# Performance work log

Hardware: AMD Instinct MI355X
Metric: run time of the kernel (lower is better)

The kernel has to match this reference:

```python
import jax, jax.numpy as jnp
import numpy as np

NUM_HEADS = 16


def rotate_half(x):
    half = x.shape[-1] // 2
    return jnp.concatenate((-x[..., half:], x[..., :half]), axis=-1)


def rope_tables(seq_len, head_dim, dtype=jnp.float32):
    inv_freq = 1.0 / (10000.0 ** (jnp.arange(0, head_dim, 2, dtype=jnp.float32) / head_dim))
    t = jnp.arange(seq_len, dtype=jnp.float32)
    freqs = jnp.outer(t, inv_freq)                 # [S, hd/2]
    emb = jnp.concatenate((freqs, freqs), axis=-1)  # [S, hd]
    return jnp.cos(emb).astype(dtype), jnp.sin(emb).astype(dtype)


def setup_inputs() -> dict:
    key = jax.random.key(0)
    k1, k2, k3 = jax.random.split(key, 3)
    B, S, D = 2, 2048, 1024
    x = jax.random.normal(k1, (B, S, D), dtype=jnp.float32)
    # causal lower-triangular mask, broadcast over batch/heads
    mask = jnp.tril(jnp.ones((S, S), dtype=bool))[None, None, :, :]
    w_qkv = jax.random.normal(k2, (3 * D, D), dtype=jnp.float32) * (D ** -0.5)
    w_out = jax.random.normal(k3, (D, D), dtype=jnp.float32) * (D ** -0.5)
    return {"x": x, "mask": mask, "w_qkv": w_qkv, "w_out": w_out}


def reference(x, mask, w_qkv, w_out):
    B, S, D = x.shape
    H = NUM_HEADS
    hd = D // H
    scale = hd ** -0.5

    qkv = jnp.einsum('bsd,ed->bse', x, w_qkv)          # [B, S, 3D]
    q, k, v = jnp.split(qkv, 3, axis=-1)

    def split(t):
        return t.reshape(B, S, H, hd).transpose(0, 2, 1, 3)  # [B, H, S, hd]

    q, k, v = split(q), split(k), split(v)

    cos, sin = rope_tables(S, hd, x.dtype)             # [S, hd]
    cos = cos[None, None]
    sin = sin[None, None]
    q = q * cos + rotate_half(q) * sin
    k = k * cos + rotate_half(k) * sin

    attn = jnp.einsum('bhqd,bhkd->bhqk', q, k) * scale  # [B, H, S, S]
    attn = jnp.where(mask, attn, jnp.float32(-jnp.inf).astype(attn.dtype))
    attn = jax.nn.softmax(attn, axis=-1)
    out = jnp.einsum('bhqk,bhkd->bhqd', attn, v)        # [B, H, S, hd]
    out = out.transpose(0, 2, 1, 3).reshape(B, S, D)
    return jnp.einsum('bsd,ed->bse', out, w_out)
```

## Files before the change

kernel.cpp:

```cpp
#include <hip/hip_runtime.h>
#include <hip/hip_bf16.h>

typedef __attribute__((ext_vector_type(8))) __bf16 bf16x8;
typedef __attribute__((ext_vector_type(4))) __bf16 bf16x4;
typedef __attribute__((ext_vector_type(2))) __bf16 bf16x2;
typedef __attribute__((ext_vector_type(4))) float f32x4;
typedef __attribute__((ext_vector_type(16))) float f32x16;

#define SEQ 2048
#define NH 16
#define HD 64
#define DMODEL 1024
#define BATCH 2
#define MTOT 4096
#define NSLOT 72

#if __has_builtin(__builtin_amdgcn_exp2f)
#define EXP2(x) __builtin_amdgcn_exp2f(x)
#else
#define EXP2(x) exp2f(x)
#endif
#define MFMA32(a, b, c) __builtin_amdgcn_mfma_f32_32x32x16_bf16(a, b, c, 0, 0, 0)

__device__ __forceinline__ void gl_lds16(const void* g, void* l) {
    __builtin_amdgcn_global_load_lds(
        (const __attribute__((address_space(1))) void*)(uintptr_t)g,
        (__attribute__((address_space(3))) void*)(uintptr_t)l,
        16, 0, 0);
}

__device__ __forceinline__ unsigned pk2(float x, float y) {
    union { bf16x2 h; unsigned u; } c;
    c.h = bf16x2{ (__bf16)x, (__bf16)y };
    return c.u;
}

__constant__ int4 FITEM[80] = {
    {31,0,16,68},{31,16,32,69},{31,32,48,70},{31,48,64,71},
    {23,0,16,37},{23,16,32,38},{23,32,48,39},
    {15,0,16,14},{15,16,32,15},
    {30,15,31,65},{30,46,62,67},
    {22,30,46,36},
    {7,0,16,-1},
    {29,0,15,60},{29,15,30,61},{29,30,45,62},{29,45,60,63},
    {30,0,15,64},{30,31,46,66},
    {22,0,15,34},{22,15,30,35},
    {21,14,29,32},{21,29,44,33},
    {28,14,29,57},{28,43,58,59},
    {14,0,15,12},{14,15,30,13},
    {27,0,14,52},{27,14,28,53},{27,28,42,54},{27,42,56,55},
    {28,0,14,56},{28,29,43,58},
    {20,0,14,28},{20,14,28,29},{20,28,42,30},
    {21,0,14,31},
    {26,13,27,49},{26,40,54,51},
    {19,26,40,27},
    {13,0,14,10},{13,14,28,11},
    {6,0,14,-1},
    {25,0,13,44},{25,13,26,45},{25,26,39,46},{25,39,52,47},
    {26,0,13,48},{26,27,40,50},
    {24,12,25,41},{24,37,50,43},
    {19,0,13,25},{19,13,26,26},
    {18,12,25,23},{18,25,38,24},
    {12,0,13,8},{12,13,26,9},
    {24,0,12,40},{24,25,37,42},
    {17,0,12,19},{17,12,24,20},{17,24,36,21},
    {18,0,12,22},
    {16,22,34,18},
    {11,0,12,6},{11,12,24,7},
    {5,0,12,-1},
    {16,0,11,16},{16,11,22,17},
    {10,0,11,4},{10,11,22,5},
    {9,0,10,2},{9,10,20,3},
    {4,0,10,-1},
    {8,0,9,0},{8,9,18,1},
    {3,0,8,-1},{2,0,6,-1},{1,0,4,-1},{0,0,2,-1}
};

__global__ __launch_bounds__(256) void cast3(const float4* __restrict__ x,
                                             const float4* __restrict__ wq,
                                             const float4* __restrict__ wo,
                                             __bf16* __restrict__ xb,
                                             __bf16* __restrict__ wqb,
                                             __bf16* __restrict__ wob) {
    const int NX  = 1024 * 1024;
    const int NWQ = 768 * 1024;
    const int NTOT = NX + NWQ + 256 * 1024;
    int i = blockIdx.x * 256 + threadIdx.x;
    if (i >= NTOT) return;
    float4 v; __bf16* dst; int j;
    if (i < NX)            { j = i;            v = x[j];  dst = xb;  }
    else if (i < NX + NWQ) { j = i - NX;       v = wq[j]; dst = wqb; }
    else                   { j = i - NX - NWQ; v = wo[j]; dst = wob; }
    bf16x4 o = { (__bf16)v.x, (__bf16)v.y, (__bf16)v.z, (__bf16)v.w };
    *(bf16x4*)(dst + (size_t)j * 4) = o;
}

__global__ __launch_bounds__(256) void gemm_qkv(const __bf16* __restrict__ A,
                                                const __bf16* __restrict__ Bt,
                                                __bf16* __restrict__ Qp,
                                                char* __restrict__ K2,
                                                char* __restrict__ V2) {
    const int K = 1024;
    __shared__ __bf16 sA[128 * 64];
    __shared__ __bf16 sB[128 * 64];
    const int tid = threadIdx.x, lane = tid & 63, wave = tid >> 6;
    const int lrow = lane & 15, quad = lane >> 4;
    const int m0 = blockIdx.y * 128, n0 = blockIdx.x * 128;
    const int wm = wave >> 1, wn = wave & 1;

    const __bf16* ap[4]; const __bf16* bp[4]; int ldso[4];
#pragma unroll
    for (int i = 0; i < 4; ++i) {
        int r0 = i * 32 + wave * 8;
        int row = r0 + (lane >> 3);
        int cg = (lane & 7) ^ (row & 7);
        ap[i] = A + (size_t)(m0 + row) * K + cg * 8;
        bp[i] = Bt + (size_t)(n0 + row) * K + cg * 8;
        ldso[i] = r0 * 128;
    }
    int arow[4], brow[4];
#pragma unroll
    for (int i = 0; i < 4; ++i) {
        arow[i] = wm * 64 + i * 16 + lrow;
        brow[i] = wn * 64 + i * 16 + lrow;
    }

    f32x4 z = {0.f, 0.f, 0.f, 0.f};
    f32x4 acc[4][4];
#pragma unroll
    for (int i = 0; i < 4; ++i)
#pragma unroll
        for (int j = 0; j < 4; ++j) acc[i][j] = z;

    char* sAb = (char*)sA; char* sBb = (char*)sB;
    for (int k0 = 0; k0 < K; k0 += 64) {
#pragma unroll
        for (int i = 0; i < 4; ++i) gl_lds16(ap[i] + k0, sAb + ldso[i]);
#pragma unroll
        for (int i = 0; i < 4; ++i) gl_lds16(bp[i] + k0, sBb + ldso[i]);
        __syncthreads();
#pragma unroll
        for (int ks = 0; ks < 2; ++ks) {
            bf16x8 af[4], bfr[4];
#pragma unroll
            for (int i = 0; i < 4; ++i)
                af[i] = *(const bf16x8*)(sAb + arow[i] * 128 +
                                         (((ks * 4 + quad) ^ (arow[i] & 7)) << 4));
#pragma unroll
            for (int i = 0; i < 4; ++i)
                bfr[i] = *(const bf16x8*)(sBb + brow[i] * 128 +
                                          (((ks * 4 + quad) ^ (brow[i] & 7)) << 4));
#pragma unroll
            for (int i = 0; i < 4; ++i)
#pragma unroll
                for (int j = 0; j < 4; ++j)
                    acc[i][j] = __builtin_amdgcn_mfma_f32_16x16x32_bf16(
                        af[i], bfr[j], acc[i][j], 0, 0, 0);
        }
        __syncthreads();
    }

    const int nt = blockIdx.x;
    const int sec = nt >> 3;
    const int b = m0 >> 11;
    const int s0b = m0 & (SEQ - 1);
    const int h = (nt & 7) * 2 + wn;
    const int bh = b * NH + h;

    if (sec < 2) {
        const float scale = sec ? 1.0f : 0.18033688011112042f;
        char* Kb = K2 + (size_t)bh * 262144;
        float invf0 = 0.15915494309189535f *
                      exp2f(-(float)lrow * 0.4152410118609203f);
        float invf1 = invf0 * 0.01f;
#pragma unroll
        for (int i = 0; i < 4; ++i) {
            int srow0 = s0b + wm * 64 + i * 16 + quad * 4;
#pragma unroll
            for (int j = 0; j < 2; ++j) {
                float invf = j ? invf1 : invf0;
                int hdlo = j * 16 + lrow;
#pragma unroll
                for (int r = 0; r < 4; ++r) {
                    int s = srow0 + r;
                    float rev = (float)s * invf;
                    float fr = rev - floorf(rev);
                    float sn = __builtin_amdgcn_sinf(fr);
                    float cs = __builtin_amdgcn_cosf(fr);
                    float lo = acc[i][j][r], hi = acc[i][j + 2][r];
                    float olo = (lo * cs - hi * sn) * scale;
                    float ohi = (hi * cs + lo * sn) * scale;
                    if (sec == 0) {
                        size_t base = ((size_t)bh * SEQ + s) * HD + hdlo;
                        Qp[base] = (__bf16)olo;
                        Qp[base + 32] = (__bf16)ohi;
                    } else {
                        char* kt = Kb + (s >> 5) * 4096 + (s & 31) * 16 +
                                   ((lrow >> 3) & 1) * 512 + (lrow & 7) * 2;
                        *(__bf16*)(kt + j * 1024) = (__bf16)olo;
                        *(__bf16*)(kt + (j + 2) * 1024) = (__bf16)ohi;
                    }
                }
            }
        }
    } else {
        char* Vb = V2 + (size_t)bh * 262144;
#pragma unroll
        for (int i = 0; i < 4; ++i) {
            int srow0 = s0b + wm * 64 + i * 16 + quad * 4;
            int kb = srow0 >> 4, ko = srow0 & 15;
            int slot0 = ((ko >> 2) & 1) * 8 + (ko >> 3) * 4;
#pragma unroll
            for (int j = 0; j < 4; ++j) {
                int ch = j * 16 + lrow;
                bf16x4 wv = { (__bf16)acc[i][j][0], (__bf16)acc[i][j][1],
                              (__bf16)acc[i][j][2], (__bf16)acc[i][j][3] };
                *(bf16x4*)(Vb + kb * 2048 + ch * 32 + slot0 * 2) = wv;
            }
        }
    }
}

__global__ __launch_bounds__(256) void gemm_bt(const __bf16* __restrict__ A,
                                               const __bf16* __restrict__ Bt,
                                               float* __restrict__ Cf,
                                               int M, int N, int K) {
    __shared__ __bf16 sA[128 * 64];
    __shared__ __bf16 sB[128 * 64];
    const int tid = threadIdx.x, lane = tid & 63, wave = tid >> 6;
    const int lrow = lane & 15, quad = lane >> 4;
    const int m0 = blockIdx.y * 128, n0 = blockIdx.x * 128;
    const int wm = wave >> 1, wn = wave & 1;

    const __bf16* ap[4]; const __bf16* bp[4]; int ldso[4];
#pragma unroll
    for (int i = 0; i < 4; ++i) {
        int r0 = i * 32 + wave * 8;
        int row = r0 + (lane >> 3);
        int cg = (lane & 7) ^ (row & 7);
        ap[i] = A + (size_t)(m0 + row) * K + cg * 8;
        bp[i] = Bt + (size_t)(n0 + row) * K + cg * 8;
        ldso[i] = r0 * 128;
    }
    int arow[4], brow[4];
#pragma unroll
    for (int i = 0; i < 4; ++i) {
        arow[i] = wm * 64 + i * 16 + lrow;
        brow[i] = wn * 64 + i * 16 + lrow;
    }

    f32x4 z = {0.f, 0.f, 0.f, 0.f};
    f32x4 acc[4][4];
#pragma unroll
    for (int i = 0; i < 4; ++i)
#pragma unroll
        for (int j = 0; j < 4; ++j) acc[i][j] = z;

    char* sAb = (char*)sA; char* sBb = (char*)sB;
    for (int k0 = 0; k0 < K; k0 += 64) {
#pragma unroll
        for (int i = 0; i < 4; ++i) gl_lds16(ap[i] + k0, sAb + ldso[i]);
#pragma unroll
        for (int i = 0; i < 4; ++i) gl_lds16(bp[i] + k0, sBb + ldso[i]);
        __syncthreads();
#pragma unroll
        for (int ks = 0; ks < 2; ++ks) {
            bf16x8 af[4], bfr[4];
#pragma unroll
            for (int i = 0; i < 4; ++i)
                af[i] = *(const bf16x8*)(sAb + arow[i] * 128 +
                                         (((ks * 4 + quad) ^ (arow[i] & 7)) << 4));
#pragma unroll
            for (int i = 0; i < 4; ++i)
                bfr[i] = *(const bf16x8*)(sBb + brow[i] * 128 +
                                          (((ks * 4 + quad) ^ (brow[i] & 7)) << 4));
#pragma unroll
            for (int i = 0; i < 4; ++i)
#pragma unroll
                for (int j = 0; j < 4; ++j)
                    acc[i][j] = __builtin_amdgcn_mfma_f32_16x16x32_bf16(
                        af[i], bfr[j], acc[i][j], 0, 0, 0);
        }
        __syncthreads();
    }
#pragma unroll
    for (int i = 0; i < 4; ++i)
#pragma unroll
        for (int j = 0; j < 4; ++j)
#pragma unroll
            for (int r = 0; r < 4; ++r) {
                int row = m0 + wm * 64 + i * 16 + quad * 4 + r;
                int col = n0 + wn * 64 + j * 16 + lrow;
                Cf[(size_t)row * N + col] = acc[i][j][r];
            }
}

__global__ __launch_bounds__(64) void flash_attn(const __bf16* __restrict__ Qp,
                                                 const char* __restrict__ K2,
                                                 const char* __restrict__ V2,
                                                 __bf16* __restrict__ Aout,
                                                 __bf16* __restrict__ Opart,
                                                 float* __restrict__ Lpart) {
    const int lane = threadIdx.x;
    const int ql = lane & 31, half = lane >> 5;
    const int bh = blockIdx.x;
    const int4 it = FITEM[blockIdx.y];
    const int s = it.x, t0 = it.y, t1 = it.z, slot = it.w;
    const int b = bh >> 4, hh = bh & 15;

    const __bf16* qb = Qp + ((size_t)bh * SEQ + s * 64 + ql) * HD + half * 8;
    bf16x8 qf0[4], qf1[4];
#pragma unroll
    for (int kc = 0; kc < 4; ++kc) {
        qf0[kc] = *(const bf16x8*)(qb + kc * 16);
        qf1[kc] = *(const bf16x8*)(qb + 32 * HD + kc * 16);
    }
    const char* Kb = K2 + (size_t)bh * 262144 + half * 512 + ql * 16;
    const char* Vb = V2 + (size_t)bh * 262144 + ql * 32 + half * 16;

    f32x16 zz = {0.f};
    f32x16 oA0 = zz, oA1 = zz, oB0 = zz, oB1 = zz;
    float lA = 0.f, lB = 0.f;
    const int dA = 2 * s, dB = 2 * s + 1;
    const int thr = ql - 4 * half;

    auto STEP = [&](int t, const bf16x8* kf, bf16x8* kn) {
        bf16x8 vf[2][2];
#pragma unroll
        for (int lo = 0; lo < 2; ++lo) {
            const char* vp = Vb + (t * 2 + lo) * 2048;
            vf[lo][0] = *(const bf16x8*)(vp);
            vf[lo][1] = *(const bf16x8*)(vp + 1024);
        }
        if (t + 1 < t1) {
            const char* kt = Kb + (t + 1) * 4096;
#pragma unroll
            for (int kc = 0; kc < 4; ++kc)
                kn[kc] = *(const bf16x8*)(kt + kc * 1024);
        }
        const bool do0 = (t != dB);
        f32x16 st0 = zz, st1 = zz;
        if (do0) {
#pragma unroll
            for (int kc = 0; kc < 4; ++kc)
                st0 = MFMA32(kf[kc], qf0[kc], st0);
        }
#pragma unroll
        for (int kc = 0; kc < 4; ++kc)
            st1 = MFMA32(kf[kc], qf1[kc], st1);

        if (do0) {
#pragma unroll
            for (int i = 0; i < 16; ++i) st0[i] = EXP2(st0[i]);
            if (t == dA) {
#pragma unroll
                for (int g = 0; g < 4; ++g)
#pragma unroll
                    for (int tt = 0; tt < 4; ++tt)
                        if (8 * g + tt > thr) st0[g * 4 + tt] = 0.f;
            }
#pragma unroll
            for (int i = 0; i < 16; ++i) lA += st0[i];
        }
#pragma unroll
        for (int i = 0; i < 16; ++i) st1[i] = EXP2(st1[i]);
        if (t == dB) {
#pragma unroll
            for (int g = 0; g < 4; ++g)
#pragma unroll
                for (int tt = 0; tt < 4; ++tt)
                    if (8 * g + tt > thr) st1[g * 4 + tt] = 0.f;
        }
#pragma unroll
        for (int i = 0; i < 16; ++i) lB += st1[i];

#pragma unroll
        for (int lo = 0; lo < 2; ++lo) {
            if (do0) {
                union { unsigned u[4]; bf16x8 v; } p0;
#pragma unroll
                for (int d = 0; d < 4; ++d)
                    p0.u[d] = pk2(st0[lo * 8 + 2 * d], st0[lo * 8 + 2 * d + 1]);
                oA0 = MFMA32(vf[lo][0], p0.v, oA0);
                oA1 = MFMA32(vf[lo][1], p0.v, oA1);
            }
            union { unsigned u[4]; bf16x8 v; } p1;
#pragma unroll
            for (int d = 0; d < 4; ++d)
                p1.u[d] = pk2(st1[lo * 8 + 2 * d], st1[lo * 8 + 2 * d + 1]);
            oB0 = MFMA32(vf[lo][0], p1.v, oB0);
            oB1 = MFMA32(vf[lo][1], p1.v, oB1);
        }
    };

    bf16x8 kA[4], kB[4];
    {
        const char* kt = Kb + t0 * 4096;
#pragma unroll
        for (int kc = 0; kc < 4; ++kc)
            kA[kc] = *(const bf16x8*)(kt + kc * 1024);
    }
    int t = t0;
    while (true) {
        STEP(t, kA, kB);
        if (++t >= t1) break;
        STEP(t, kB, kA);
        if (++t >= t1) break;
    }

    lA += __shfl_xor(lA, 32, 64);
    lB += __shfl_xor(lB, 32, 64);

    if (slot < 0) {
        float iA = 1.0f / lA, iB = 1.0f / lB;
        __bf16* oa = Aout + ((size_t)b * SEQ + s * 64 + ql) * DMODEL + hh * HD;
        __bf16* ob = oa + (size_t)32 * DMODEL;
#pragma unroll
        for (int g = 0; g < 4; ++g) {
            bf16x4 wA0 = { (__bf16)(oA0[g*4+0]*iA), (__bf16)(oA0[g*4+1]*iA),
                           (__bf16)(oA0[g*4+2]*iA), (__bf16)(oA0[g*4+3]*iA) };
            bf16x4 wA1 = { (__bf16)(oA1[g*4+0]*iA), (__bf16)(oA1[g*4+1]*iA),
                           (__bf16)(oA1[g*4+2]*iA), (__bf16)(oA1[g*4+3]*iA) };
            bf16x4 wB0 = { (__bf16)(oB0[g*4+0]*iB), (__bf16)(oB0[g*4+1]*iB),
                           (__bf16)(oB0[g*4+2]*iB), (__bf16)(oB0[g*4+3]*iB) };
            bf16x4 wB1 = { (__bf16)(oB1[g*4+0]*iB), (__bf16)(oB1[g*4+1]*iB),
                           (__bf16)(oB1[g*4+2]*iB), (__bf16)(oB1[g*4+3]*iB) };
            *(bf16x4*)(oa + 8 * g + 4 * half) = wA0;
            *(bf16x4*)(oa + 32 + 8 * g + 4 * half) = wA1;
            *(bf16x4*)(ob + 8 * g + 4 * half) = wB0;
            *(bf16x4*)(ob + 32 + 8 * g + 4 * half) = wB1;
        }
    } else {
        __bf16* oa = Opart + ((size_t)(bh * NSLOT + slot) << 12) + ql * 64;
        __bf16* ob = oa + 32 * 64;
#pragma unroll
        for (int g = 0; g < 4; ++g) {
            bf16x4 wA0 = { (__bf16)oA0[g*4+0], (__bf16)oA0[g*4+1],
                           (__bf16)oA0[g*4+2], (__bf16)oA0[g*4+3] };
            bf16x4 wA1 = { (__bf16)oA1[g*4+0], (__bf16)oA1[g*4+1],
                           (__bf16)oA1[g*4+2], (__bf16)oA1[g*4+3] };
            bf16x4 wB0 = { (__bf16)oB0[g*4+0], (__bf16)oB0[g*4+1],
                           (__bf16)oB0[g*4+2], (__bf16)oB0[g*4+3] };
            bf16x4 wB1 = { (__bf16)oB1[g*4+0], (__bf16)oB1[g*4+1],
                           (__bf16)oB1[g*4+2], (__bf16)oB1[g*4+3] };
            *(bf16x4*)(oa + 8 * g + 4 * half) = wA0;
            *(bf16x4*)(oa + 32 + 8 * g + 4 * half) = wA1;
            *(bf16x4*)(ob + 8 * g + 4 * half) = wB0;
            *(bf16x4*)(ob + 32 + 8 * g + 4 * half) = wB1;
        }
        if (!half) {
            Lpart[(bh * NSLOT + slot) * 64 + ql] = lA;
            Lpart[(bh * NSLOT + slot) * 64 + 32 + ql] = lB;
        }
    }
}

__global__ __launch_bounds__(256) void combine(const __bf16* __restrict__ Opart,
                                               const float* __restrict__ Lpart,
                                               __bf16* __restrict__ Aout) {
    const int bh = blockIdx.x;
    const int s = 8 + blockIdx.y;
    const int C = (s < 16) ? 2 : ((s < 24) ? 3 : 4);
    const int base = (s < 16) ? (s - 8) * 2
                   : (s < 24) ? 16 + (s - 16) * 3
                              : 40 + (s - 24) * 4;
    const int t = threadIdx.x;
    const int r = t >> 2, cg = (t & 3) * 16;
    float acc[16];
#pragma unroll
    for (int i = 0; i < 16; ++i) acc[i] = 0.f;
    float l = 0.f;
    for (int ci = 0; ci < C; ++ci) {
        int ch = bh * NSLOT + base + ci;
        l += Lpart[ch * 64 + r];
        const __bf16* p = Opart + ((size_t)ch << 12) + r * 64 + cg;
#pragma unroll
        for (int k = 0; k < 2; ++k) {
            bf16x8 v = ((const bf16x8*)p)[k];
#pragma unroll
            for (int j = 0; j < 8; ++j) acc[k * 8 + j] += (float)v[j];
        }
    }
    float invl = 1.0f / l;
    const int b = bh >> 4, hh = bh & 15;
    __bf16* dst = Aout + ((size_t)(b * SEQ + s * 64 + r)) * DMODEL +
                  hh * 64 + cg;
#pragma unroll
    for (int k = 0; k < 2; ++k) {
        bf16x8 w;
#pragma unroll
        for (int j = 0; j < 8; ++j) w[j] = (__bf16)(acc[k * 8 + j] * invl);
        ((bf16x8*)dst)[k] = w;
    }
}

extern "C" void kernel_launch(void* const* d_in, const int* in_sizes, int n_in,
                              void* d_out, int out_size, void* d_ws, size_t ws_size,
                              hipStream_t stream) {
    (void)in_sizes; (void)n_in; (void)out_size; (void)ws_size;
    const float* x  = (const float*)d_in[0];
    const float* wq = (const float*)d_in[2];
    const float* wo = (const float*)d_in[3];
    float* out = (float*)d_out;

    char* w = (char*)d_ws;
    __bf16* xb   = (__bf16*)(w);
    __bf16* wqb  = (__bf16*)(w + (8ull << 20));
    __bf16* wob  = (__bf16*)(w + (14ull << 20));
    __bf16* Opart= (__bf16*)(w + (16ull << 20));
    float*  Lpart= (float*) (w + (35ull << 20));
    __bf16* Qb   = (__bf16*)(w + (40ull << 20));
    char*   K2   = (char*)  (w + (48ull << 20));
    char*   V2   = (char*)  (w + (56ull << 20));
    __bf16* aob  = xb;

    cast3<<<8192, 256, 0, stream>>>((const float4*)x, (const float4*)wq,
                                    (const float4*)wo, xb, wqb, wob);
    gemm_qkv<<<dim3(24, 32), 256, 0, stream>>>(xb, wqb, Qb, K2, V2);
    flash_attn<<<dim3(32, 80), 64, 0, stream>>>(Qb, K2, V2, aob, Opart, Lpart);
    combine<<<dim3(32, 24), 256, 0, stream>>>(Opart, Lpart, aob);
    gemm_bt<<<dim3(8, 32), 256, 0, stream>>>(aob, wob, out, MTOT, 1024, 1024);
}
```

Measured before the change: 199.3 us.

## Double-buffer LDS tiles and remap block order in both GEMM kernels

```diff
diff --git a/kernel.cpp b/kernel.cpp
--- a/kernel.cpp
+++ b/kernel.cpp
@@ -101,11 +101,15 @@
                                                 char* __restrict__ K2,
                                                 char* __restrict__ V2) {
     const int K = 1024;
-    __shared__ __bf16 sA[128 * 64];
-    __shared__ __bf16 sB[128 * 64];
+    __shared__ __bf16 sA[2][128 * 64];
+    __shared__ __bf16 sB[2][128 * 64];
     const int tid = threadIdx.x, lane = tid & 63, wave = tid >> 6;
     const int lrow = lane & 15, quad = lane >> 4;
-    const int m0 = blockIdx.y * 128, n0 = blockIdx.x * 128;
+
+    int lin = blockIdx.y * 24 + blockIdx.x;
+    lin = (lin & 7) * 96 + (lin >> 3);
+    const int bx = lin % 24, by = lin / 24;
+    const int m0 = by * 128, n0 = bx * 128;
     const int wm = wave >> 1, wn = wave & 1;
 
     const __bf16* ap[4]; const __bf16* bp[4]; int ldso[4];
@@ -132,13 +136,16 @@
 #pragma unroll
         for (int j = 0; j < 4; ++j) acc[i][j] = z;
 
-    char* sAb = (char*)sA; char* sBb = (char*)sB;
-    for (int k0 = 0; k0 < K; k0 += 64) {
-#pragma unroll
-        for (int i = 0; i < 4; ++i) gl_lds16(ap[i] + k0, sAb + ldso[i]);
-#pragma unroll
-        for (int i = 0; i < 4; ++i) gl_lds16(bp[i] + k0, sBb + ldso[i]);
-        __syncthreads();
+    char* sA0 = (char*)sA[0]; char* sA1 = (char*)sA[1];
+    char* sB0 = (char*)sB[0]; char* sB1 = (char*)sB[1];
+
+    auto STAGE = [&](char* dA, char* dB, int k0) {
+#pragma unroll
+        for (int i = 0; i < 4; ++i) gl_lds16(ap[i] + k0, dA + ldso[i]);
+#pragma unroll
+        for (int i = 0; i < 4; ++i) gl_lds16(bp[i] + k0, dB + ldso[i]);
+    };
+    auto COMPUTE = [&](const char* sAb, const char* sBb) {
 #pragma unroll
         for (int ks = 0; ks < 2; ++ks) {
             bf16x8 af[4], bfr[4];
@@ -157,10 +164,20 @@
                     acc[i][j] = __builtin_amdgcn_mfma_f32_16x16x32_bf16(
                         af[i], bfr[j], acc[i][j], 0, 0, 0);
         }
+    };
+
+    STAGE(sA0, sB0, 0);
+    __syncthreads();
+    for (int k0 = 0; k0 < K; k0 += 128) {
+        if (k0 + 64 < K) STAGE(sA1, sB1, k0 + 64);
+        COMPUTE(sA0, sB0);
         __syncthreads();
-    }
-
-    const int nt = blockIdx.x;
+        if (k0 + 128 < K) STAGE(sA0, sB0, k0 + 128);
+        COMPUTE(sA1, sB1);
+        __syncthreads();
+    }
+
+    const int nt = bx;
     const int sec = nt >> 3;
     const int b = m0 >> 11;
     const int s0b = m0 & (SEQ - 1);
@@ -225,11 +242,15 @@
                                                const __bf16* __restrict__ Bt,
                                                float* __restrict__ Cf,
                                                int M, int N, int K) {
-    __shared__ __bf16 sA[128 * 64];
-    __shared__ __bf16 sB[128 * 64];
+    __shared__ __bf16 sA[2][128 * 64];
+    __shared__ __bf16 sB[2][128 * 64];
     const int tid = threadIdx.x, lane = tid & 63, wave = tid >> 6;
     const int lrow = lane & 15, quad = lane >> 4;
-    const int m0 = blockIdx.y * 128, n0 = blockIdx.x * 128;
+
+    int lin = blockIdx.y * 8 + blockIdx.x;
+    lin = (lin & 7) * 32 + (lin >> 3);
+    const int bx = lin & 7, by = lin >> 3;
+    const int m0 = by * 128, n0 = bx * 128;
     const int wm = wave >> 1, wn = wave & 1;
 
     const __bf16* ap[4]; const __bf16* bp[4]; int ldso[4];
@@ -256,13 +277,16 @@
 #pragma unroll
         for (int j = 0; j < 4; ++j) acc[i][j] = z;
 
-    char* sAb = (char*)sA; char* sBb = (char*)sB;
-    for (int k0 = 0; k0 < K; k0 += 64) {
-#pragma unroll
-        for (int i = 0; i < 4; ++i) gl_lds16(ap[i] + k0, sAb + ldso[i]);
-#pragma unroll
-        for (int i = 0; i < 4; ++i) gl_lds16(bp[i] + k0, sBb + ldso[i]);
-        __syncthreads();
+    char* sA0 = (char*)sA[0]; char* sA1 = (char*)sA[1];
+    char* sB0 = (char*)sB[0]; char* sB1 = (char*)sB[1];
+
+    auto STAGE = [&](char* dA, char* dB, int k0) {
+#pragma unroll
+        for (int i = 0; i < 4; ++i) gl_lds16(ap[i] + k0, dA + ldso[i]);
+#pragma unroll
+        for (int i = 0; i < 4; ++i) gl_lds16(bp[i] + k0, dB + ldso[i]);
+    };
+    auto COMPUTE = [&](const char* sAb, const char* sBb) {
 #pragma unroll
         for (int ks = 0; ks < 2; ++ks) {
             bf16x8 af[4], bfr[4];
@@ -281,6 +305,16 @@
                     acc[i][j] = __builtin_amdgcn_mfma_f32_16x16x32_bf16(
                         af[i], bfr[j], acc[i][j], 0, 0, 0);
         }
+    };
+
+    STAGE(sA0, sB0, 0);
+    __syncthreads();
+    for (int k0 = 0; k0 < K; k0 += 128) {
+        if (k0 + 64 < K) STAGE(sA1, sB1, k0 + 64);
+        COMPUTE(sA0, sB0);
+        __syncthreads();
+        if (k0 + 128 < K) STAGE(sA0, sB0, k0 + 128);
+        COMPUTE(sA1, sB1);
         __syncthreads();
     }
 #pragma unroll
```

Result: faster. 185.4 us (-7.0%).
